# Kernel optimization log

Hardware: AMD Instinct MI355X
Metric: run time of the kernel (lower is better)

The kernel has to match this reference:

```python
import jax, jax.numpy as jnp
import numpy as np

K = 8
NEG = -1e16


def setup_inputs() -> dict:
    key = jax.random.key(0)
    inputs = jax.random.normal(key, (1048576, 64), dtype=jnp.float32)
    return {"inputs": inputs}


def reference(inputs) -> jnp.ndarray:
    depth = inputs.shape[1]
    # top-k along last axis (values unused; only indices form the mask)
    _, top_k_indices = jax.lax.top_k(inputs, K)            # [N, K]
    # sum of one-hots -> membership mask [N, depth]
    one_hot = jax.nn.one_hot(top_k_indices, depth, dtype=inputs.dtype)  # [N, K, depth]
    mask = jnp.sum(one_hot, axis=1)                        # [N, depth]
    sparse_inputs = jnp.where(mask > 0.0, inputs, jnp.full_like(inputs, NEG))
    return jax.nn.softmax(sparse_inputs, axis=1)
```

## Files before the change

kernel.cpp:

```cpp
#include <hip/hip_runtime.h>
#include <math.h>


#define D4 16
#define ROWS 16
#define TILE_F4 (ROWS * D4)
#define WAVES 4
#define THREADS (WAVES * 64)

typedef float nfloat4 __attribute__((ext_vector_type(4)));

#define LVL(ti) { const float _hi = fmaxf(ti, _a); _a = fminf(ti, _a); ti = _hi; }
#define INSERT(x) { float _a = (x); \
    LVL(t0) LVL(t1) LVL(t2) LVL(t3) LVL(t4) LVL(t5) LVL(t6) \
    t7 = fmaxf(t7, _a); }

#define CE(a, b) { const float _hi = fmaxf(a, b); b = fminf(a, b); a = _hi; }

#define PROC(x, o) { \
    const int _kgt = ((x) > thr); \
    const int _keq = ((x) == thr) & (quota > 0); \
    quota -= _keq; \
    (o) = (_kgt | _keq) ? __expf((x) - m) * inv : 0.0f; }

__device__ __forceinline__ void gload_lds16(const void* g, void* l) {
    __builtin_amdgcn_global_load_lds(
        (__attribute__((address_space(1))) void*)(g),
        (__attribute__((address_space(3))) void*)(l),
        16, 0, 0);
}

__global__ __launch_bounds__(THREADS, 8)
void topk_softmax_kernel(const float* __restrict__ in,
                         float* __restrict__ out,
                         int ntiles)
{
    __shared__ float4 tile_[WAVES][TILE_F4];

    const int lane = threadIdx.x & 63;
    const int wid  = threadIdx.x >> 6;
    const int w = blockIdx.x * WAVES + wid;
    if (w >= ntiles) return;
    float4* tile = tile_[wid];

    const float4* __restrict__ p = reinterpret_cast<const float4*>(in) + (long long)w * TILE_F4;
    float4* __restrict__ q       = reinterpret_cast<float4*>(out)      + (long long)w * TILE_F4;

    const int g = lane >> 4;
    const int s = lane & 15;

    #pragma unroll
    for (int c = 0; c < 4; ++c) {
        const int r = c * 4 + g;
        gload_lds16(p + r * 16 + (s ^ r), tile + c * 64);
    }
    asm volatile("s_waitcnt vmcnt(0)" ::: "memory");

    const int r2 = lane & 15;
    const int h  = lane >> 4;
    const int qb = h * 4;
    float t0 = -INFINITY, t1 = -INFINITY, t2 = -INFINITY, t3 = -INFINITY,
          t4 = -INFINITY, t5 = -INFINITY, t6 = -INFINITY, t7 = -INFINITY;
    #pragma unroll
    for (int j = 0; j < 4; ++j) {
        const float4 v = tile[r2 * 16 + ((qb + j) ^ r2)];
        INSERT(v.x) INSERT(v.y) INSERT(v.z) INSERT(v.w)
    }

    const float pa0 = __shfl_xor(t0, 16), pa1 = __shfl_xor(t1, 16),
                pa2 = __shfl_xor(t2, 16), pa3 = __shfl_xor(t3, 16),
                pa4 = __shfl_xor(t4, 16), pa5 = __shfl_xor(t5, 16),
                pa6 = __shfl_xor(t6, 16), pa7 = __shfl_xor(t7, 16);
    float c0 = fmaxf(t0, pa7), c1 = fmaxf(t1, pa6), c2 = fmaxf(t2, pa5),
          c3 = fmaxf(t3, pa4), c4 = fmaxf(t4, pa3), c5 = fmaxf(t5, pa2),
          c6 = fmaxf(t6, pa1), c7 = fmaxf(t7, pa0);
    CE(c0, c4) CE(c1, c5) CE(c2, c6) CE(c3, c7)
    CE(c0, c2) CE(c1, c3) CE(c4, c6) CE(c5, c7)
    CE(c0, c1) CE(c2, c3) CE(c4, c5) CE(c6, c7)

    const float pb0 = __shfl_xor(c0, 32), pb1 = __shfl_xor(c1, 32),
                pb2 = __shfl_xor(c2, 32), pb3 = __shfl_xor(c3, 32),
                pb4 = __shfl_xor(c4, 32), pb5 = __shfl_xor(c5, 32),
                pb6 = __shfl_xor(c6, 32), pb7 = __shfl_xor(c7, 32);
    const float f0 = fmaxf(c0, pb7), f1 = fmaxf(c1, pb6), f2 = fmaxf(c2, pb5),
                f3 = fmaxf(c3, pb4), f4 = fmaxf(c4, pb3), f5 = fmaxf(c5, pb2),
                f6 = fmaxf(c6, pb1), f7 = fmaxf(c7, pb0);

    const float m   = fmaxf(c0, pb0);
    const float thr = fminf(fminf(fminf(f0, f1), fminf(f2, f3)),
                            fminf(fminf(f4, f5), fminf(f6, f7)));
    const int cnt_gt = (f0 > thr) + (f1 > thr) + (f2 > thr) + (f3 > thr) +
                       (f4 > thr) + (f5 > thr) + (f6 > thr) + (f7 > thr);
    const float sum = __expf(f0 - m) + __expf(f1 - m) + __expf(f2 - m) + __expf(f3 - m) +
                      __expf(f4 - m) + __expf(f5 - m) + __expf(f6 - m) + __expf(f7 - m);
    const float inv = 1.0f / sum;

    const int ce = (t0 == thr) + (t1 == thr) + (t2 == thr) + (t3 == thr) +
                   (t4 == thr) + (t5 == thr) + (t6 == thr) + (t7 == thr);
    const int e1 = __shfl_xor(ce, 16);
    const int e2 = __shfl_xor(ce, 32);
    const int e3 = __shfl_xor(e1, 32);
    const int a0 = (h == 0) ? ce : (h == 1) ? e1 : (h == 2) ? e2 : e3;
    const int a1 = (h == 1) ? ce : (h == 0) ? e1 : (h == 3) ? e2 : e3;
    const int a2 = (h == 2) ? ce : (h == 3) ? e1 : (h == 0) ? e2 : e3;
    const int pre = (h > 0 ? a0 : 0) + (h > 1 ? a1 : 0) + (h > 2 ? a2 : 0);
    int quota = 8 - cnt_gt - pre;

    #pragma unroll
    for (int j = 0; j < 4; ++j) {
        const int slot = r2 * 16 + ((qb + j) ^ r2);
        const float4 v = tile[slot];
        float4 o;
        PROC(v.x, o.x) PROC(v.y, o.y) PROC(v.z, o.z) PROC(v.w, o.w)
        tile[slot] = o;
    }
    asm volatile("s_waitcnt lgkmcnt(0)" ::: "memory");

    #pragma unroll
    for (int c = 0; c < 4; ++c) {
        const int r = c * 4 + g;
        const float4 o = tile[r * 16 + (s ^ r)];
        nfloat4 no; no.x = o.x; no.y = o.y; no.z = o.z; no.w = o.w;
        __builtin_nontemporal_store(no,
            reinterpret_cast<nfloat4*>(q + c * 64 + lane));
    }
}

__global__ __launch_bounds__(64)
void topk_softmax_tail(const float* __restrict__ in, float* __restrict__ out,
                       long long row0, long long nrows)
{
    const long long row = row0 + threadIdx.x;
    if (row >= nrows) return;
    const float4* __restrict__ p = reinterpret_cast<const float4*>(in) + row * D4;
    float4* __restrict__ q       = reinterpret_cast<float4*>(out)      + row * D4;
    float4 v[D4];
    #pragma unroll
    for (int c = 0; c < D4; ++c) v[c] = p[c];
    float t0 = -INFINITY, t1 = -INFINITY, t2 = -INFINITY, t3 = -INFINITY,
          t4 = -INFINITY, t5 = -INFINITY, t6 = -INFINITY, t7 = -INFINITY;
    #pragma unroll
    for (int c = 0; c < D4; ++c) {
        INSERT(v[c].x) INSERT(v[c].y) INSERT(v[c].z) INSERT(v[c].w)
    }
    const float thr = t7;
    const float m   = t0;
    int quota = 8 - ((t0 > thr) + (t1 > thr) + (t2 > thr) + (t3 > thr) +
                     (t4 > thr) + (t5 > thr) + (t6 > thr));
    const float sum = __expf(t0 - m) + __expf(t1 - m) + __expf(t2 - m) + __expf(t3 - m) +
                      __expf(t4 - m) + __expf(t5 - m) + __expf(t6 - m) + __expf(t7 - m);
    const float inv = 1.0f / sum;
    #pragma unroll
    for (int c = 0; c < D4; ++c) {
        float4 o;
        PROC(v[c].x, o.x) PROC(v[c].y, o.y) PROC(v[c].z, o.z) PROC(v[c].w, o.w)
        q[c] = o;
    }
}

extern "C" void kernel_launch(void* const* d_in, const int* in_sizes, int n_in,
                              void* d_out, int out_size, void* d_ws, size_t ws_size,
                              hipStream_t stream) {
    const float* in = (const float*)d_in[0];
    float* out = (float*)d_out;
    const long long nrows = in_sizes[0] / 64;
    const int ntiles = (int)(nrows / ROWS);
    const long long rem = nrows - (long long)ntiles * ROWS;

    if (ntiles > 0) {
        const int nblocks = (ntiles + WAVES - 1) / WAVES;
        topk_softmax_kernel<<<nblocks, THREADS, 0, stream>>>(in, out, ntiles);
    }
    if (rem > 0) {
        topk_softmax_tail<<<1, 64, 0, stream>>>(in, out, (long long)ntiles * ROWS, nrows);
    }
}
```

Baseline: 82.80 us.

## Use med3 top-k insertion, log-sum-exp bias, and tie-free fast path

Replaces the compare-exchange insertion chain with v_med3-based parallel insertion, so each element costs one max plus seven med3 ops instead of a serial max/min chain. Folds the softmax normalization into a bias B = m + log(sum), removing the per-element multiply by the reciprocal. Adds a wave-uniform fast path that uses a simple >= threshold test when a packed shuffle reduction shows no ties at the threshold. A slow path recomputes equality counts from the actual values for tie handling. It adds a logf, an extra wave-level vote and some code-size and branching overhead, and exp(x-B) can differ slightly numerically from exp(x-m)*inv.

```diff
diff --git a/kernel.cpp b/kernel.cpp
--- a/kernel.cpp
+++ b/kernel.cpp
@@ -10,13 +10,30 @@
 
 typedef float nfloat4 __attribute__((ext_vector_type(4)));
 
+#define INS(xx) { \
+    const float _x = (xx); \
+    const float n0 = fmaxf(t0, _x); \
+    const float n1 = __builtin_amdgcn_fmed3f(t0, t1, _x); \
+    const float n2 = __builtin_amdgcn_fmed3f(t1, t2, _x); \
+    const float n3 = __builtin_amdgcn_fmed3f(t2, t3, _x); \
+    const float n4 = __builtin_amdgcn_fmed3f(t3, t4, _x); \
+    const float n5 = __builtin_amdgcn_fmed3f(t4, t5, _x); \
+    const float n6 = __builtin_amdgcn_fmed3f(t5, t6, _x); \
+    const float n7 = __builtin_amdgcn_fmed3f(t6, t7, _x); \
+    t0 = n0; t1 = n1; t2 = n2; t3 = n3; t4 = n4; t5 = n5; t6 = n6; t7 = n7; }
+
+#define CE(a, b) { const float _hi = fmaxf(a, b); b = fminf(a, b); a = _hi; }
+
+#define PROCF(x, o) { (o) = ((x) >= thr) ? __expf((x) - B) : 0.0f; }
+#define PROCS(x, o) { \
+    const int _k = ((x) == thr) & (quota > 0); \
+    quota -= _k; \
+    (o) = (((x) > thr) | _k) ? __expf((x) - B) : 0.0f; }
+
 #define LVL(ti) { const float _hi = fmaxf(ti, _a); _a = fminf(ti, _a); ti = _hi; }
 #define INSERT(x) { float _a = (x); \
     LVL(t0) LVL(t1) LVL(t2) LVL(t3) LVL(t4) LVL(t5) LVL(t6) \
     t7 = fmaxf(t7, _a); }
-
-#define CE(a, b) { const float _hi = fmaxf(a, b); b = fminf(a, b); a = _hi; }
-
 #define PROC(x, o) { \
     const int _kgt = ((x) > thr); \
     const int _keq = ((x) == thr) & (quota > 0); \
@@ -64,7 +81,7 @@
     #pragma unroll
     for (int j = 0; j < 4; ++j) {
         const float4 v = tile[r2 * 16 + ((qb + j) ^ r2)];
-        INSERT(v.x) INSERT(v.y) INSERT(v.z) INSERT(v.w)
+        INS(v.x) INS(v.y) INS(v.z) INS(v.w)
     }
 
     const float pa0 = __shfl_xor(t0, 16), pa1 = __shfl_xor(t1, 16),
@@ -93,26 +110,50 @@
                        (f4 > thr) + (f5 > thr) + (f6 > thr) + (f7 > thr);
     const float sum = __expf(f0 - m) + __expf(f1 - m) + __expf(f2 - m) + __expf(f3 - m) +
                       __expf(f4 - m) + __expf(f5 - m) + __expf(f6 - m) + __expf(f7 - m);
-    const float inv = 1.0f / sum;
-
-    const int ce = (t0 == thr) + (t1 == thr) + (t2 == thr) + (t3 == thr) +
-                   (t4 == thr) + (t5 == thr) + (t6 == thr) + (t7 == thr);
-    const int e1 = __shfl_xor(ce, 16);
-    const int e2 = __shfl_xor(ce, 32);
-    const int e3 = __shfl_xor(e1, 32);
-    const int a0 = (h == 0) ? ce : (h == 1) ? e1 : (h == 2) ? e2 : e3;
-    const int a1 = (h == 1) ? ce : (h == 0) ? e1 : (h == 3) ? e2 : e3;
-    const int a2 = (h == 2) ? ce : (h == 3) ? e1 : (h == 0) ? e2 : e3;
-    const int pre = (h > 0 ? a0 : 0) + (h > 1 ? a1 : 0) + (h > 2 ? a2 : 0);
-    int quota = 8 - cnt_gt - pre;
-
-    #pragma unroll
-    for (int j = 0; j < 4; ++j) {
-        const int slot = r2 * 16 + ((qb + j) ^ r2);
-        const float4 v = tile[slot];
-        float4 o;
-        PROC(v.x, o.x) PROC(v.y, o.y) PROC(v.z, o.z) PROC(v.w, o.w)
-        tile[slot] = o;
+    const float B = m + __logf(sum);
+    const int qrow = 8 - cnt_gt;
+
+    const int ce8 = (t0 == thr) + (t1 == thr) + (t2 == thr) + (t3 == thr) +
+                    (t4 == thr) + (t5 == thr) + (t6 == thr) + (t7 == thr);
+    const int pack = ce8 | ((t7 == thr) ? 256 : 0);
+    const int v1 = pack + __shfl_xor(pack, 16);
+    const int v2 = v1 + __shfl_xor(v1, 32);
+    const bool slow = ((v2 & 255) != qrow) | (v2 >> 8);
+
+    if (!__any(slow)) {
+        #pragma unroll
+        for (int j = 0; j < 4; ++j) {
+            const int slot = r2 * 16 + ((qb + j) ^ r2);
+            const float4 v = tile[slot];
+            float4 o;
+            PROCF(v.x, o.x) PROCF(v.y, o.y) PROCF(v.z, o.z) PROCF(v.w, o.w)
+            tile[slot] = o;
+        }
+    } else {
+        float4 vv[4];
+        int my_eq = 0;
+        #pragma unroll
+        for (int j = 0; j < 4; ++j) {
+            vv[j] = tile[r2 * 16 + ((qb + j) ^ r2)];
+            my_eq += (vv[j].x == thr) + (vv[j].y == thr) +
+                     (vv[j].z == thr) + (vv[j].w == thr);
+        }
+        const int e1 = __shfl_xor(my_eq, 16);
+        const int e2 = __shfl_xor(my_eq, 32);
+        const int e3 = __shfl_xor(e1, 32);
+        const int a0 = (h == 0) ? my_eq : (h == 1) ? e1 : (h == 2) ? e2 : e3;
+        const int a1 = (h == 1) ? my_eq : (h == 0) ? e1 : (h == 3) ? e2 : e3;
+        const int a2 = (h == 2) ? my_eq : (h == 3) ? e1 : (h == 0) ? e2 : e3;
+        const int pre = (h > 0 ? a0 : 0) + (h > 1 ? a1 : 0) + (h > 2 ? a2 : 0);
+        int quota = slow ? (qrow - pre) : 999;
+        #pragma unroll
+        for (int j = 0; j < 4; ++j) {
+            const int slot = r2 * 16 + ((qb + j) ^ r2);
+            float4 o;
+            PROCS(vv[j].x, o.x) PROCS(vv[j].y, o.y)
+            PROCS(vv[j].z, o.z) PROCS(vv[j].w, o.w)
+            tile[slot] = o;
+        }
     }
     asm volatile("s_waitcnt lgkmcnt(0)" ::: "memory");
 
```

After: 83.53 us. About the same (+0.9%).
